# Kernel tuning notes

Hardware: AMD Instinct MI355X
Metric: run time of the kernel (lower is better)

Reference implementation:

```python
import jax, jax.numpy as jnp
import numpy as np

OUT, IN = 11008, 4096  # LLaMA-7B FFN up-projection


def _unpack(packed, shape):
    """Unpack 2-bit fields (4 ternary values per byte, stored as q+1 in {0,1,2})."""
    shifts = jnp.arange(4, dtype=packed.dtype) * 2
    vals = (packed[:, None] >> shifts) & 3            # [n_bytes, 4]
    n = shape[0] * shape[1]
    q = vals.reshape(-1)[:n].astype(jnp.float32) - 1.0  # back to {-1,0,1}
    return q.reshape(shape)


def _pack(q):
    """Pack ternary int values {-1,0,1} -> 2-bit fields, 4 per byte."""
    flat = (q + 1).reshape(-1)
    pad = (-flat.shape[0]) % 4
    flat = jnp.pad(flat, (0, pad))
    groups = flat.reshape(-1, 4)
    weights = (jnp.int32(1) << (jnp.arange(4, dtype=jnp.int32) * 2))
    return jnp.sum(groups * weights, axis=1).astype(jnp.int32)


def setup_inputs() -> dict:
    key = jax.random.key(0)
    kx, kw = jax.random.split(key)
    x = jax.random.normal(kx, (4, 2048, IN), dtype=jnp.float32)
    # build a realistic weight, then absmean-quantize it (per output row)
    W = jax.random.normal(kw, (OUT, IN), dtype=jnp.float32) * 0.02
    weight_scale = jnp.mean(jnp.abs(W), axis=1, keepdims=True)  # [OUT, 1]
    q = jnp.clip(jnp.round(W / weight_scale), -1.0, 1.0).astype(jnp.int32)
    packed_weight = _pack(q)  # [OUT*IN/4] int32 bytes
    return {"x": x, "packed_weight": packed_weight, "weight_scale": weight_scale}


def reference(x, packed_weight, weight_scale):
    # unpack ternary weights, dequantize via per-row scale, dense GEMM
    W = _unpack(packed_weight, (OUT, IN)) * weight_scale  # [OUT, IN] fp32
    return jnp.einsum('bsi,oi->bso', x, W)
```

## Files before the change

kernel.cpp:

```cpp
#include <hip/hip_runtime.h>
#include <hip/hip_bf16.h>


#define M_DIM 8192
#define N_DIM 11008
#define K_DIM 4096
#define BM 128
#define BN 256
#define KT32 32
#define NB_N 43
#define NWG 2752

#define XBF_BYTES ((size_t)M_DIM * K_DIM * 2)
#define BT_BYTES  ((size_t)N_DIM * K_DIM / 4)
#define WS_NEED   (XBF_BYTES + BT_BYTES)

typedef __attribute__((ext_vector_type(8))) short bf16x8;
typedef __attribute__((ext_vector_type(4))) float f32x4;

__device__ inline unsigned int bf16b(float f) {
  union { __hip_bfloat16 h; unsigned short u; } cv;
  cv.h = __float2bfloat16(f);
  return (unsigned int)cv.u;
}

__device__ __forceinline__ void gload_lds16(const void* g, void* l) {
  __builtin_amdgcn_global_load_lds(
      (const __attribute__((address_space(1))) unsigned int*)g,
      (__attribute__((address_space(3))) unsigned int*)l, 16, 0, 0);
}

#define XCVT_BLOCKS 16384
#define PACK_BLOCKS 5504
__global__ __launch_bounds__(256)
void xcvt_kernel(const float* __restrict__ X, unsigned short* __restrict__ Xbf) {
  const size_t i8 = ((size_t)blockIdx.x * 256 + threadIdx.x) * 8;
  float4 a = *(const float4*)(X + i8);
  float4 c = *(const float4*)(X + i8 + 4);
  uint4 o;
  o.x = bf16b(a.x) | (bf16b(a.y) << 16);
  o.y = bf16b(a.z) | (bf16b(a.w) << 16);
  o.z = bf16b(c.x) | (bf16b(c.y) << 16);
  o.w = bf16b(c.z) | (bf16b(c.w) << 16);
  *(uint4*)(Xbf + i8) = o;
}

__global__ __launch_bounds__(256)
void btight_kernel(const int* __restrict__ PW, unsigned char* __restrict__ Bt) {
  const size_t i8 = ((size_t)blockIdx.x * 256 + threadIdx.x) * 8;
  int4 p = *(const int4*)(PW + i8);
  int4 q = *(const int4*)(PW + i8 + 4);
  uint2 o;
  o.x = (unsigned)(p.x & 255) | ((unsigned)(p.y & 255) << 8) |
        ((unsigned)(p.z & 255) << 16) | ((unsigned)(p.w & 255) << 24);
  o.y = (unsigned)(q.x & 255) | ((unsigned)(q.y & 255) << 8) |
        ((unsigned)(q.z & 255) << 16) | ((unsigned)(q.w & 255) << 24);
  *(uint2*)(Bt + i8) = o;
}

__global__ __launch_bounds__(256, 2)
void qlin_bk128_kernel(const unsigned short* __restrict__ Xbf,
                       const unsigned char* __restrict__ Bt,
                       const float* __restrict__ SC, float* __restrict__ OUT) {
  __shared__ unsigned short As[2][2][8192];
  __shared__ unsigned char  Bs[2][2][4096];

  const int tid = threadIdx.x;
  const int lane = tid & 63;
  const int w = tid >> 6;

  const int wg = blockIdx.x;
  const int swz = (wg & 7) * (NWG / 8) + (wg >> 3);
  const int bm = swz / NB_N;
  const int bn = swz - bm * NB_N;

  const int l3 = lane >> 3;
  const char* ab0 = (const char*)Xbf +
      (size_t)(bm * BM + w * 32 + l3) * (K_DIM * 2) + ((lane & 7) ^ l3) * 16;
  const char* bb = (const char*)Bt + (size_t)(bn * BN + w * 64 + lane) * (K_DIM / 4);

#define STAGE(IDX, KT_) do {                                                   \
    _Pragma("unroll")                                                          \
    for (int h = 0; h < 2; ++h) {                                              \
      unsigned short* ad_ = &As[IDX][h][w * 2048];                             \
      const char* as_ = ab0 + (KT_) * 256 + h * 128;                           \
      gload_lds16(as_,           ad_);                                         \
      gload_lds16(as_ + 65536,   ad_ + 512);                                   \
      gload_lds16(as_ + 131072,  ad_ + 1024);                                  \
      gload_lds16(as_ + 196608,  ad_ + 1536);                                  \
      gload_lds16(bb + (KT_) * 32 + h * 16, &Bs[IDX][h][w * 1024]);            \
    }                                                                          \
  } while (0)

  f32x4 acc[8][4];
#pragma unroll
  for (int i = 0; i < 8; ++i)
#pragma unroll
    for (int j = 0; j < 4; ++j) acc[i][j] = (f32x4){0.f, 0.f, 0.f, 0.f};

  const int l4 = lane >> 4;
  const int axor = lane & 7;
  const int arow = (lane & 15) * 128;
  const int hb = l4 >> 1;
  const unsigned hoff = (unsigned)(l4 & 1) * 16;
  const int rbase = (w * 64 + (lane & 15)) * 16 + hb * 4;

#define COMPUTE(B_) do {                                                        \
    _Pragma("unroll")                                                           \
    for (int kk = 0; kk < 4; ++kk) {                                            \
      const int h_ = kk >> 1;                                                   \
      const int kp_ = kk & 1;                                                   \
      const char* asb_ = (const char*)&As[B_][h_][0];                           \
      const unsigned char* bsb_ = &Bs[B_][h_][0];                               \
      bf16x8 af[8];                                                             \
      _Pragma("unroll")                                                         \
      for (int m = 0; m < 8; ++m)                                               \
        af[m] = *(const bf16x8*)(asb_ + m * 2048 + arow +                       \
                                 (((kp_ * 4 + l4) ^ axor) << 4));               \
      _Pragma("unroll")                                                         \
      for (int n = 0; n < 4; ++n) {                                             \
        const unsigned d = *(const unsigned*)(bsb_ + rbase + n * 256 + kp_ * 8); \
        const unsigned w16 = (d >> hoff) & 0xFFFFu;                             \
        const unsigned u = w16 | (w16 << 14);                                   \
        union { uint4 s; bf16x8 v; } bfr;                                       \
        bfr.s.x = ((u << 14) & 0xC000C000u) + 0x40004000u;                      \
        bfr.s.y = ((u << 10) & 0xC000C000u) + 0x40004000u;                      \
        bfr.s.z = ((u << 6)  & 0xC000C000u) + 0x40004000u;                      \
        bfr.s.w = ((u << 2)  & 0xC000C000u) + 0x40004000u;                      \
        _Pragma("unroll")                                                       \
        for (int m = 0; m < 8; ++m)                                             \
          acc[m][n] = __builtin_amdgcn_mfma_f32_16x16x32_bf16(af[m], bfr.v,     \
                                                              acc[m][n], 0, 0, 0); \
      }                                                                         \
    }                                                                           \
  } while (0)

  STAGE(0, 0);
  int cur = 0;
  for (int kt = 0; kt < KT32 - 1; ++kt) {
    STAGE(cur ^ 1, kt + 1);
    asm volatile("s_waitcnt vmcnt(10)" ::: "memory");
    __builtin_amdgcn_s_barrier();
    COMPUTE(cur);
    asm volatile("s_waitcnt lgkmcnt(0)" ::: "memory");
    __builtin_amdgcn_s_barrier();
    cur ^= 1;
  }
  asm volatile("s_waitcnt vmcnt(0)" ::: "memory");
  __builtin_amdgcn_s_barrier();
  COMPUTE(cur);
#undef STAGE
#undef COMPUTE

  const int gc0 = bn * BN + w * 64 + (lane & 15);
  const int gr0 = bm * BM + (l4 << 2);
  float sc[4];
#pragma unroll
  for (int n = 0; n < 4; ++n) sc[n] = -0.5f * SC[gc0 + n * 16];
#pragma unroll
  for (int m = 0; m < 8; ++m)
#pragma unroll
    for (int n = 0; n < 4; ++n)
#pragma unroll
      for (int r = 0; r < 4; ++r)
        OUT[(size_t)(gr0 + m * 16 + r) * N_DIM + gc0 + n * 16] = acc[m][n][r] * sc[n];
}

#define BSTRIDE 20
__global__ __launch_bounds__(256, 2)
void qlin_fused_kernel(const float* __restrict__ X, const int* __restrict__ PW,
                       const float* __restrict__ SC, float* __restrict__ OUT) {
  __shared__ unsigned short Asf[128 * 64];
  __shared__ unsigned char Bp[256 * BSTRIDE];

  const int tid = threadIdx.x;
  const int wg = blockIdx.x;
  const int swz = (wg & 7) * (NWG / 8) + (wg >> 3);
  const int bm = swz / NB_N;
  const int bn = swz - bm * NB_N;

  const int lane = tid & 63;
  const int wave = tid >> 6;
  const int wr = wave >> 1;
  const int wc = wave & 1;

  const int arow = tid >> 3;
  const int ac8  = tid & 7;
  const float* xptr = X + (size_t)(bm * 128 + arow) * K_DIM + ac8 * 8;
  const unsigned int aswz = ((unsigned)arow & 7u) << 4;

  const int bc  = tid & 3;
  const int br0 = tid >> 2;
  const int* pwptr = PW + (size_t)(bn * 256 + br0) * (K_DIM / 4) + bc * 4;
  const int bwoff = (bc & 1) * 8 + (bc >> 1) * 2;

  f32x4 acc[4][8];
#pragma unroll
  for (int i = 0; i < 4; ++i)
#pragma unroll
    for (int j = 0; j < 8; ++j) acc[i][j] = (f32x4){0.f, 0.f, 0.f, 0.f};

  float4 av[4][2];
  int4 bv[4];
#pragma unroll
  for (int j = 0; j < 4; ++j) {
    av[j][0] = *(const float4*)(xptr + (size_t)(32 * j) * K_DIM);
    av[j][1] = *(const float4*)(xptr + (size_t)(32 * j) * K_DIM + 4);
  }
#pragma unroll
  for (int j = 0; j < 4; ++j)
    bv[j] = *(const int4*)(pwptr + (size_t)(64 * j) * (K_DIM / 4));

  for (int kt = 0; kt < 64; ++kt) {
    __syncthreads();
#pragma unroll
    for (int j = 0; j < 4; ++j) {
      uint4 wv;
      wv.x = bf16b(av[j][0].x) | (bf16b(av[j][0].y) << 16);
      wv.y = bf16b(av[j][0].z) | (bf16b(av[j][0].w) << 16);
      wv.z = bf16b(av[j][1].x) | (bf16b(av[j][1].y) << 16);
      wv.w = bf16b(av[j][1].z) | (bf16b(av[j][1].w) << 16);
      *(uint4*)((char*)Asf + (arow + 32 * j) * 128 + (((unsigned)ac8 * 16u) ^ aswz)) = wv;
    }
#pragma unroll
    for (int j = 0; j < 4; ++j) {
      const unsigned int ulo = ((unsigned)bv[j].x & 255u) | (((unsigned)bv[j].y & 255u) << 8);
      const unsigned int uhi = ((unsigned)bv[j].z & 255u) | (((unsigned)bv[j].w & 255u) << 8);
      unsigned char* dst = Bp + (br0 + 64 * j) * BSTRIDE + bwoff;
      *(unsigned short*)(dst)     = (unsigned short)ulo;
      *(unsigned short*)(dst + 4) = (unsigned short)uhi;
    }
    __syncthreads();

    if (kt + 1 < 64) {
#pragma unroll
      for (int j = 0; j < 4; ++j) {
        av[j][0] = *(const float4*)(xptr + (kt + 1) * 64 + (size_t)(32 * j) * K_DIM);
        av[j][1] = *(const float4*)(xptr + (kt + 1) * 64 + (size_t)(32 * j) * K_DIM + 4);
      }
#pragma unroll
      for (int j = 0; j < 4; ++j)
        bv[j] = *(const int4*)(pwptr + (kt + 1) * 16 + (size_t)(64 * j) * (K_DIM / 4));
    }

    const int bh = lane >> 4;
    const int bcol0 = wc * 128 + (lane & 15);
    unsigned int d[8];
#pragma unroll
    for (int n = 0; n < 8; ++n)
      d[n] = *(const unsigned int*)(Bp + (bcol0 + n * 16) * BSTRIDE + bh * 4);

    const unsigned int rswz = ((unsigned)lane & 7u) << 4;
#pragma unroll
    for (int kk = 0; kk < 2; ++kk) {
      bf16x8 af[4];
      const unsigned int coff = (((unsigned)(kk * 4 + (lane >> 4))) * 16u) ^ rswz;
#pragma unroll
      for (int m = 0; m < 4; ++m)
        af[m] = *(const bf16x8*)((const char*)Asf + (wr * 64 + m * 16 + (lane & 15)) * 128 + coff);
#pragma unroll
      for (int n = 0; n < 8; ++n) {
        const unsigned int w16 = kk ? (d[n] >> 16) : (d[n] & 0xFFFFu);
        const unsigned int u = w16 | (w16 << 14);
        union { uint4 s; bf16x8 v; } bfr;
        bfr.s.x = ((u << 14) & 0xC000C000u) + 0x40004000u;
        bfr.s.y = ((u << 10) & 0xC000C000u) + 0x40004000u;
        bfr.s.z = ((u << 6)  & 0xC000C000u) + 0x40004000u;
        bfr.s.w = ((u << 2)  & 0xC000C000u) + 0x40004000u;
#pragma unroll
        for (int m = 0; m < 4; ++m)
          acc[m][n] = __builtin_amdgcn_mfma_f32_16x16x32_bf16(af[m], bfr.v, acc[m][n], 0, 0, 0);
      }
    }
  }

  const int gc0 = bn * 256 + wc * 128 + (lane & 15);
  const int gr0 = bm * 128 + wr * 64 + ((lane >> 4) << 2);
  float sc[8];
#pragma unroll
  for (int n = 0; n < 8; ++n) sc[n] = -0.5f * SC[gc0 + n * 16];
#pragma unroll
  for (int m = 0; m < 4; ++m)
#pragma unroll
    for (int n = 0; n < 8; ++n)
#pragma unroll
      for (int r = 0; r < 4; ++r)
        OUT[(size_t)(gr0 + m * 16 + r) * N_DIM + gc0 + n * 16] = acc[m][n][r] * sc[n];
}

extern "C" void kernel_launch(void* const* d_in, const int* in_sizes, int n_in,
                              void* d_out, int out_size, void* d_ws, size_t ws_size,
                              hipStream_t stream) {
  const float* x  = (const float*)d_in[0];
  const int*   pw = (const int*)d_in[1];
  const float* sc = (const float*)d_in[2];
  float* out = (float*)d_out;
  (void)in_sizes; (void)n_in; (void)out_size;

  if (ws_size >= WS_NEED) {
    unsigned short* xbf = (unsigned short*)d_ws;
    unsigned char* bt = (unsigned char*)d_ws + XBF_BYTES;
    xcvt_kernel<<<dim3(XCVT_BLOCKS), dim3(256), 0, stream>>>(x, xbf);
    btight_kernel<<<dim3(PACK_BLOCKS), dim3(256), 0, stream>>>(pw, bt);
    qlin_bk128_kernel<<<dim3(NWG), dim3(256), 0, stream>>>(xbf, bt, sc, out);
  } else {
    qlin_fused_kernel<<<dim3(NWG), dim3(256), 0, stream>>>(x, pw, sc, out);
  }
}
```

Before: 645.8 us.

## Switch GEMM to 32x32x16 MFMA with tile-ordered packed weight layout

Replaces the 16x16x32 bf16 MFMA tiling with 32x32x16 MFMAs, so each wave holds a 4x2 grid of 32x32 accumulators. The weight-packing pre-kernel now writes the 2-bit weights in a per-tile, k-slice-major layout, so each stage's B tile is one contiguous block and each lane's fragment is a single 32-bit LDS read. The aim is fewer MFMA issues and fewer LDS reads per FLOP. In exchange, the output store pattern changes to the 32x32 accumulator layout, and the reorder kernel does strided scattered writes.

```diff
diff --git a/kernel.cpp b/kernel.cpp
--- a/kernel.cpp
+++ b/kernel.cpp
@@ -17,6 +17,7 @@
 
 typedef __attribute__((ext_vector_type(8))) short bf16x8;
 typedef __attribute__((ext_vector_type(4))) float f32x4;
+typedef __attribute__((ext_vector_type(16))) float f32x16;
 
 __device__ inline unsigned int bf16b(float f) {
   union { __hip_bfloat16 h; unsigned short u; } cv;
@@ -31,7 +32,6 @@
 }
 
 #define XCVT_BLOCKS 16384
-#define PACK_BLOCKS 5504
 __global__ __launch_bounds__(256)
 void xcvt_kernel(const float* __restrict__ X, unsigned short* __restrict__ Xbf) {
   const size_t i8 = ((size_t)blockIdx.x * 256 + threadIdx.x) * 8;
@@ -45,25 +45,29 @@
   *(uint4*)(Xbf + i8) = o;
 }
 
+#define BRE_BLOCKS 1376
 __global__ __launch_bounds__(256)
-void btight_kernel(const int* __restrict__ PW, unsigned char* __restrict__ Bt) {
-  const size_t i8 = ((size_t)blockIdx.x * 256 + threadIdx.x) * 8;
-  int4 p = *(const int4*)(PW + i8);
-  int4 q = *(const int4*)(PW + i8 + 4);
-  uint2 o;
-  o.x = (unsigned)(p.x & 255) | ((unsigned)(p.y & 255) << 8) |
-        ((unsigned)(p.z & 255) << 16) | ((unsigned)(p.w & 255) << 24);
-  o.y = (unsigned)(q.x & 255) | ((unsigned)(q.y & 255) << 8) |
-        ((unsigned)(q.z & 255) << 16) | ((unsigned)(q.w & 255) << 24);
-  *(uint2*)(Bt + i8) = o;
+void breorder_kernel(const int* __restrict__ PW, unsigned char* __restrict__ Bt) {
+  const int ti = blockIdx.x * 256 + threadIdx.x;
+  const int row = ti & 255;
+  const int kt  = (ti >> 8) & 31;
+  const int bn  = ti >> 13;
+  const int* src = PW + (size_t)(bn * 256 + row) * (K_DIM / 4) + kt * 32;
+  unsigned* dst = (unsigned*)Bt + (size_t)bn * 65536 + kt * 2048 + row;
+#pragma unroll
+  for (int ks = 0; ks < 8; ++ks) {
+    int4 v = *(const int4*)(src + ks * 4);
+    dst[ks * 256] = ((unsigned)v.x & 255u) | (((unsigned)v.y & 255u) << 8) |
+                    (((unsigned)v.z & 255u) << 16) | (((unsigned)v.w & 255u) << 24);
+  }
 }
 
 __global__ __launch_bounds__(256, 2)
-void qlin_bk128_kernel(const unsigned short* __restrict__ Xbf,
-                       const unsigned char* __restrict__ Bt,
-                       const float* __restrict__ SC, float* __restrict__ OUT) {
+void qlin_mm32_kernel(const unsigned short* __restrict__ Xbf,
+                      const unsigned char* __restrict__ Bt,
+                      const float* __restrict__ SC, float* __restrict__ OUT) {
   __shared__ unsigned short As[2][2][8192];
-  __shared__ unsigned char  Bs[2][2][4096];
+  __shared__ unsigned char  Bs[2][8192];
 
   const int tid = threadIdx.x;
   const int lane = tid & 63;
@@ -77,7 +81,7 @@
   const int l3 = lane >> 3;
   const char* ab0 = (const char*)Xbf +
       (size_t)(bm * BM + w * 32 + l3) * (K_DIM * 2) + ((lane & 7) ^ l3) * 16;
-  const char* bb = (const char*)Bt + (size_t)(bn * BN + w * 64 + lane) * (K_DIM / 4);
+  const char* bimg = (const char*)Bt + (size_t)(bn * KT32) * 8192;
 
 #define STAGE(IDX, KT_) do {                                                   \
     _Pragma("unroll")                                                          \
@@ -88,50 +92,59 @@
       gload_lds16(as_ + 65536,   ad_ + 512);                                   \
       gload_lds16(as_ + 131072,  ad_ + 1024);                                  \
       gload_lds16(as_ + 196608,  ad_ + 1536);                                  \
-      gload_lds16(bb + (KT_) * 32 + h * 16, &Bs[IDX][h][w * 1024]);            \
     }                                                                          \
+    const char* bs_ = bimg + (size_t)(KT_) * 8192 + w * 2048 + lane * 16;      \
+    unsigned char* bd_ = &Bs[IDX][w * 2048];                                   \
+    gload_lds16(bs_,          bd_);                                            \
+    gload_lds16(bs_ + 1024,   bd_ + 1024);                                     \
   } while (0)
 
-  f32x4 acc[8][4];
-#pragma unroll
-  for (int i = 0; i < 8; ++i)
-#pragma unroll
-    for (int j = 0; j < 4; ++j) acc[i][j] = (f32x4){0.f, 0.f, 0.f, 0.f};
-
-  const int l4 = lane >> 4;
-  const int axor = lane & 7;
-  const int arow = (lane & 15) * 128;
-  const int hb = l4 >> 1;
-  const unsigned hoff = (unsigned)(l4 & 1) * 16;
-  const int rbase = (w * 64 + (lane & 15)) * 16 + hb * 4;
+  f32x16 acc[4][2];
+#pragma unroll
+  for (int i = 0; i < 4; ++i)
+#pragma unroll
+    for (int j = 0; j < 2; ++j)
+#pragma unroll
+      for (int r = 0; r < 16; ++r) acc[i][j][r] = 0.f;
+
+  const int l31 = lane & 31;
+  const int l5 = lane >> 5;
+  const int a7 = lane & 7;
+  const unsigned hoff = (unsigned)l5 * 16;
+  const int arow32 = l31 * 128;
 
 #define COMPUTE(B_) do {                                                        \
     _Pragma("unroll")                                                           \
-    for (int kk = 0; kk < 4; ++kk) {                                            \
-      const int h_ = kk >> 1;                                                   \
-      const int kp_ = kk & 1;                                                   \
-      const char* asb_ = (const char*)&As[B_][h_][0];                           \
-      const unsigned char* bsb_ = &Bs[B_][h_][0];                               \
-      bf16x8 af[8];                                                             \
+    for (int ks = 0; ks < 8; ++ks) {                                            \
+      const int kh_ = ks >> 2;                                                  \
+      const int kl_ = ks & 3;                                                   \
+      const char* asb_ = (const char*)&As[B_][kh_][0];                          \
+      const unsigned char* bsb_ = &Bs[B_][0];                                   \
+      bf16x8 af[4];                                                             \
       _Pragma("unroll")                                                         \
-      for (int m = 0; m < 8; ++m)                                               \
-        af[m] = *(const bf16x8*)(asb_ + m * 2048 + arow +                       \
-                                 (((kp_ * 4 + l4) ^ axor) << 4));               \
+      for (int mt = 0; mt < 4; ++mt)                                            \
+        af[mt] = *(const bf16x8*)(asb_ + mt * 4096 + arow32 +                   \
+                                  (((kl_ * 2 + l5) ^ a7) << 4));                \
+      bf16x8 bfr[2];                                                            \
       _Pragma("unroll")                                                         \
-      for (int n = 0; n < 4; ++n) {                                             \
-        const unsigned d = *(const unsigned*)(bsb_ + rbase + n * 256 + kp_ * 8); \
+      for (int nt = 0; nt < 2; ++nt) {                                          \
+        const unsigned d = *(const unsigned*)(bsb_ + ks * 1024 +                \
+                                              (w * 64 + nt * 32 + l31) * 4);    \
         const unsigned w16 = (d >> hoff) & 0xFFFFu;                             \
         const unsigned u = w16 | (w16 << 14);                                   \
-        union { uint4 s; bf16x8 v; } bfr;                                       \
-        bfr.s.x = ((u << 14) & 0xC000C000u) + 0x40004000u;                      \
-        bfr.s.y = ((u << 10) & 0xC000C000u) + 0x40004000u;                      \
-        bfr.s.z = ((u << 6)  & 0xC000C000u) + 0x40004000u;                      \
-        bfr.s.w = ((u << 2)  & 0xC000C000u) + 0x40004000u;                      \
+        union { uint4 s; bf16x8 v; } t;                                         \
+        t.s.x = ((u << 14) & 0xC000C000u) + 0x40004000u;                        \
+        t.s.y = ((u << 10) & 0xC000C000u) + 0x40004000u;                        \
+        t.s.z = ((u << 6)  & 0xC000C000u) + 0x40004000u;                        \
+        t.s.w = ((u << 2)  & 0xC000C000u) + 0x40004000u;                        \
+        bfr[nt] = t.v;                                                          \
+      }                                                                         \
+      _Pragma("unroll")                                                         \
+      for (int mt = 0; mt < 4; ++mt)                                            \
         _Pragma("unroll")                                                       \
-        for (int m = 0; m < 8; ++m)                                             \
-          acc[m][n] = __builtin_amdgcn_mfma_f32_16x16x32_bf16(af[m], bfr.v,     \
-                                                              acc[m][n], 0, 0, 0); \
-      }                                                                         \
+        for (int nt = 0; nt < 2; ++nt)                                          \
+          acc[mt][nt] = __builtin_amdgcn_mfma_f32_32x32x16_bf16(                \
+              af[mt], bfr[nt], acc[mt][nt], 0, 0, 0);                           \
     }                                                                           \
   } while (0)
 
@@ -152,18 +165,20 @@
 #undef STAGE
 #undef COMPUTE
 
-  const int gc0 = bn * BN + w * 64 + (lane & 15);
-  const int gr0 = bm * BM + (l4 << 2);
-  float sc[4];
-#pragma unroll
-  for (int n = 0; n < 4; ++n) sc[n] = -0.5f * SC[gc0 + n * 16];
-#pragma unroll
-  for (int m = 0; m < 8; ++m)
-#pragma unroll
-    for (int n = 0; n < 4; ++n)
-#pragma unroll
-      for (int r = 0; r < 4; ++r)
-        OUT[(size_t)(gr0 + m * 16 + r) * N_DIM + gc0 + n * 16] = acc[m][n][r] * sc[n];
+#pragma unroll
+  for (int nt = 0; nt < 2; ++nt) {
+    const int gc = bn * BN + w * 64 + nt * 32 + l31;
+    const float s = -0.5f * SC[gc];
+#pragma unroll
+    for (int mt = 0; mt < 4; ++mt) {
+      const int gr0 = bm * BM + mt * 32 + 4 * l5;
+#pragma unroll
+      for (int reg = 0; reg < 16; ++reg) {
+        const int row = gr0 + (reg & 3) + 8 * (reg >> 2);
+        OUT[(size_t)row * N_DIM + gc] = acc[mt][nt][reg] * s;
+      }
+    }
+  }
 }
 
 #define BSTRIDE 20
@@ -301,8 +316,8 @@
     unsigned short* xbf = (unsigned short*)d_ws;
     unsigned char* bt = (unsigned char*)d_ws + XBF_BYTES;
     xcvt_kernel<<<dim3(XCVT_BLOCKS), dim3(256), 0, stream>>>(x, xbf);
-    btight_kernel<<<dim3(PACK_BLOCKS), dim3(256), 0, stream>>>(pw, bt);
-    qlin_bk128_kernel<<<dim3(NWG), dim3(256), 0, stream>>>(xbf, bt, sc, out);
+    breorder_kernel<<<dim3(BRE_BLOCKS), dim3(256), 0, stream>>>(pw, bt);
+    qlin_mm32_kernel<<<dim3(NWG), dim3(256), 0, stream>>>(xbf, bt, sc, out);
   } else {
     qlin_fused_kernel<<<dim3(NWG), dim3(256), 0, stream>>>(x, pw, sc, out);
   }
```

Result: faster. 630.1 us (-2.4%).
